# Kernel tuning notes

Measured on AMD Instinct MI355X. Metric: run time of the kernel, lower is better.

The kernel has to match this reference:

```python
import jax, jax.numpy as jnp
import numpy as np

B, D, H, NC = 4096, 128, 4, 10
HD = D // H
EPS = 1e-5


def _ln(x, g, b):
    m = jnp.mean(x, axis=-1, keepdims=True)
    v = jnp.var(x, axis=-1, keepdims=True)
    return (x - m) * jax.lax.rsqrt(v + EPS) * g + b


def _mlp(x, w1, b1, w2, b2):
    h = jax.nn.gelu(x @ w1.T + b1, approximate=False)  # nn.GELU default = exact erf
    return h @ w2.T + b2


def setup_inputs():
    key = jax.random.key(0)
    ks = iter(jax.random.split(key, 40))
    w = lambda *s: jax.random.normal(next(ks), s, dtype=jnp.float32) * 0.02
    inp = {
        'coords': jax.random.uniform(next(ks), (B, 2), dtype=jnp.float32),
        'labels': jax.random.randint(next(ks), (B,), 0, NC),
        'ce_w': w(D, 2), 'ce_b': w(D),
        'emb': w(NC, D),
        'sa_in_w': w(3 * D, D), 'sa_in_b': w(3 * D),
        'sa_out_w': w(D, D), 'sa_out_b': w(D),
        'n1_g': jnp.ones(D), 'n1_b': jnp.zeros(D),
        'm1_w1': w(4 * D, D), 'm1_b1': w(4 * D), 'm1_w2': w(D, 4 * D), 'm1_b2': w(D),
        'n2_g': jnp.ones(D), 'n2_b': jnp.zeros(D),
        'ca_in_w': w(3 * D, D), 'ca_in_b': w(3 * D),
        'ca_out_w': w(D, D), 'ca_out_b': w(D),
        'n3_g': jnp.ones(D), 'n3_b': jnp.zeros(D),
        'm2_w1': w(4 * D, D), 'm2_b1': w(4 * D), 'm2_w2': w(D, 4 * D), 'm2_b2': w(D),
        'n4_g': jnp.ones(D), 'n4_b': jnp.zeros(D),
        'fin_w': w(1, D), 'fin_b': w(1),
    }
    return inp


def reference(coords, labels, ce_w, ce_b, emb, sa_in_w, sa_in_b, sa_out_w, sa_out_b,
              n1_g, n1_b, m1_w1, m1_b1, m1_w2, m1_b2, n2_g, n2_b,
              ca_in_w, ca_in_b, ca_out_w, ca_out_b, n3_g, n3_b,
              m2_w1, m2_b1, m2_w2, m2_b2, n4_g, n4_b, fin_w, fin_b):
    # --- vectorized positional encoding (original loops over batch) ---
    div = 10000.0 ** (2.0 * jnp.arange(D // 2, dtype=jnp.float32) / D)  # [D/2]
    pe_sin = jnp.sin(coords[:, 0:1] / div)  # even slots
    pe_cos = jnp.cos(coords[:, 1:2] / div)  # odd slots
    pe = jnp.stack([pe_sin, pe_cos], axis=-1).reshape(B, D)

    x = coords @ ce_w.T + ce_b + pe  # [B, D]

    # --- self-attention: seq_len = B, batch = 1 (torch seq-first semantics) ---
    qkv = x @ sa_in_w.T + sa_in_b  # [B, 3D]
    q, k, v = jnp.split(qkv, 3, axis=-1)
    q = q.reshape(B, H, HD); k = k.reshape(B, H, HD); v = v.reshape(B, H, HD)
    scores = jnp.einsum('qhd,khd->hqk', q, k) / jnp.sqrt(jnp.float32(HD))  # [H,B,B]
    attn = jax.nn.softmax(scores, axis=-1)
    sa = jnp.einsum('hqk,khd->qhd', attn, v).reshape(B, D) @ sa_out_w.T + sa_out_b

    x = _ln(x + sa, n1_g, n1_b)
    x = _ln(x + _mlp(x, m1_w1, m1_b1, m1_w2, m1_b2), n2_g, n2_b)

    # --- cross-attention: per-sample q_len = kv_len = 1 -> softmax over a
    # single key is exactly 1, so output = out_proj(v_proj(label_emb)) ---
    lab = emb[labels]  # [B, D]
    wv = ca_in_w[2 * D:]; bv = ca_in_b[2 * D:]
    ca = (lab @ wv.T + bv) @ ca_out_w.T + ca_out_b

    x = _ln(x + ca, n3_g, n3_b)
    x = _ln(x + _mlp(x, m2_w1, m2_b1, m2_w2, m2_b2), n4_g, n4_b)

    return jax.nn.sigmoid(x @ fin_w.T + fin_b)  # [B, 1]
```

## Files before the change

kernel.cpp:

```cpp
#include <hip/hip_runtime.h>
#include <hip/hip_bf16.h>


typedef __bf16 bf16_t;
typedef __bf16 bf16x8 __attribute__((ext_vector_type(8)));
typedef __bf16 bf16x4 __attribute__((ext_vector_type(4)));
typedef __bf16 bf16x2 __attribute__((ext_vector_type(2)));
typedef float  f32x4  __attribute__((ext_vector_type(4)));
typedef float  f32x2  __attribute__((ext_vector_type(2)));

__device__ __forceinline__ f32x4 mfma16(bf16x8 a, bf16x8 b, f32x4 c) {
  return __builtin_amdgcn_mfma_f32_16x16x32_bf16(a, b, c, 0, 0, 0);
}

__global__ __launch_bounds__(256) void k_init(const float* __restrict__ coords,
                                              const float* __restrict__ ce_w,
                                              const float* __restrict__ ce_b,
                                              float* __restrict__ xf,
                                              bf16_t* __restrict__ xb,
                                              const float* __restrict__ s0,
                                              const float* __restrict__ s1,
                                              const float* __restrict__ s2,
                                              const float* __restrict__ s3,
                                              const float* __restrict__ s4,
                                              const float* __restrict__ s5,
                                              bf16_t* __restrict__ wdst,
                                              const float* __restrict__ emb,
                                              const float* __restrict__ wvp,
                                              const float* __restrict__ bvp,
                                              const float* __restrict__ cow,
                                              const float* __restrict__ cob,
                                              float* __restrict__ tab) {
  const int bid = blockIdx.x;
  const int tid = threadIdx.x;
  if (bid < 2048) {
    int row = bid * 2 + (tid >> 7);
    int d   = tid & 127;
    float c0 = coords[row * 2 + 0];
    float c1 = coords[row * 2 + 1];
    int   j  = d >> 1;
    float inv = exp2f(-0.20762050593045953f * (float)j);
    float pe  = (d & 1) ? cosf(c1 * inv) : sinf(c0 * inv);
    float x = c0 * ce_w[2 * d] + c1 * ce_w[2 * d + 1] + ce_b[d] + pe;
    xf[(size_t)row * 128 + d] = x;
    xb[(size_t)row * 128 + d] = (bf16_t)x;
  } else if (bid < 2368) {
    int i = (bid - 2048) * 256 + tid;
    const float* src; int off;
    if      (i < 12288) { src = s0; off = i; }
    else if (i < 16384) { src = s1; off = i - 12288; }
    else if (i < 32768) { src = s2; off = i - 16384; }
    else if (i < 49152) { src = s3; off = i - 32768; }
    else if (i < 65536) { src = s4; off = i - 49152; }
    else                { src = s5; off = i - 65536; }
    f32x4 v = *(const f32x4*)(src + (size_t)off * 4);
    bf16x4 o = {(bf16_t)v[0], (bf16_t)v[1], (bf16_t)v[2], (bf16_t)v[3]};
    *(bf16x4*)(wdst + (size_t)i * 4) = o;
  } else {
    __shared__ float embs[10][128];
    __shared__ float t1[10][128];
    for (int i = tid; i < 1280; i += 256) embs[i >> 7][i & 127] = emb[i];
    __syncthreads();
    for (int o = tid; o < 1280; o += 256) {
      int c = o >> 7, n = o & 127;
      float acc = bvp[n];
      const float* wr = wvp + n * 128;
      for (int k2 = 0; k2 < 128; k2++) acc += embs[c][k2] * wr[k2];
      t1[c][n] = acc;
    }
    __syncthreads();
    for (int o = tid; o < 1280; o += 256) {
      int c = o >> 7, dd = o & 127;
      float acc = cob[dd];
      const float* wr = cow + dd * 128;
      for (int n = 0; n < 128; n++) acc += t1[c][n] * wr[n];
      tab[o] = acc;
    }
  }
}

enum { EPI_BF16 = 1, EPI_GELU_BF16 = 2 };

template <int K, int EPI>
__global__ __launch_bounds__(256) void k_gemm(const bf16_t* __restrict__ X,
                                              const bf16_t* __restrict__ Wb,
                                              const float* __restrict__ bias,
                                              bf16_t* __restrict__ outB,
                                              bf16_t* __restrict__ vTout,
                                              int N) {
  const int tid  = threadIdx.x;
  const int lane = tid & 63;
  const int wv   = tid >> 6;
  const int l15  = lane & 15;
  const int quad = lane >> 4;
  const int xbase = blockIdx.x * 64 + (wv >> 1) * 32;
  const int wbase = blockIdx.y * 64 + (wv & 1) * 32;

  const bf16_t* wr0 = Wb + (size_t)(wbase + l15) * K + quad * 8;
  const bf16_t* xr0 = X  + (size_t)(xbase + l15) * K + quad * 8;

  f32x4 acc[2][2];
  const f32x4 zero4 = {0.f, 0.f, 0.f, 0.f};
  for (int i = 0; i < 2; i++)
    for (int t = 0; t < 2; t++) acc[i][t] = zero4;

#pragma unroll 4
  for (int kk = 0; kk < K; kk += 32) {
    bf16x8 a0 = *(const bf16x8*)(wr0 + kk);
    bf16x8 a1 = *(const bf16x8*)(wr0 + 16 * K + kk);
    bf16x8 b0 = *(const bf16x8*)(xr0 + kk);
    bf16x8 b1 = *(const bf16x8*)(xr0 + 16 * K + kk);
    acc[0][0] = mfma16(a0, b0, acc[0][0]);
    acc[0][1] = mfma16(a0, b1, acc[0][1]);
    acc[1][0] = mfma16(a1, b0, acc[1][0]);
    acc[1][1] = mfma16(a1, b1, acc[1][1]);
  }

  f32x4 bv[2];
  bv[0] = *(const f32x4*)(bias + wbase + quad * 4);
  bv[1] = *(const f32x4*)(bias + wbase + 16 + quad * 4);
#pragma unroll
  for (int t = 0; t < 2; t++) {
    int row = xbase + t * 16 + l15;
#pragma unroll
    for (int i = 0; i < 2; i++) {
      int col0 = wbase + i * 16 + quad * 4;
      f32x4 v = acc[i][t] + bv[i];
      if (EPI == EPI_GELU_BF16) {
#pragma unroll
        for (int r = 0; r < 4; r++)
          v[r] = 0.5f * v[r] * (1.0f + erff(v[r] * 0.70710678118654752f));
      }
      bf16x4 o = {(bf16_t)v[0], (bf16_t)v[1], (bf16_t)v[2], (bf16_t)v[3]};
      *(bf16x4*)(outB + (size_t)row * N + col0) = o;
      if (vTout && col0 >= 256) {
#pragma unroll
        for (int r = 0; r < 4; r++)
          vTout[(size_t)(col0 - 256 + r) * 4096 + row] = (bf16_t)v[r];
      }
    }
  }
}

template <int K, int MODE>
__global__ __launch_bounds__(256) void k_gemmln(const bf16_t* __restrict__ X,
                                                const bf16_t* __restrict__ Wb,
                                                const float* __restrict__ bias,
                                                const float* __restrict__ resid,
                                                const float* __restrict__ g1,
                                                const float* __restrict__ b1,
                                                const int* __restrict__ labels,
                                                const float* __restrict__ tab,
                                                const float* __restrict__ g2,
                                                const float* __restrict__ b2,
                                                const float* __restrict__ fw,
                                                const float* __restrict__ fb,
                                                float* __restrict__ xf_out,
                                                bf16_t* __restrict__ xb_out,
                                                float* __restrict__ out) {
  __shared__ float red[2][64][2];

  const int tid  = threadIdx.x;
  const int lane = tid & 63;
  const int wv   = tid >> 6;
  const int l15  = lane & 15;
  const int quad = lane >> 4;
  const int rhalf = wv >> 1, chalf = wv & 1;
  const int rb = blockIdx.x * 64 + rhalf * 32;
  const int cb = chalf * 64;

  const bf16_t* xr0 = X  + (size_t)(rb + l15) * K + quad * 8;
  const bf16_t* wr0 = Wb + (size_t)(cb + l15) * K + quad * 8;

  f32x4 acc[2][4];
  const f32x4 zero4 = {0.f, 0.f, 0.f, 0.f};
  for (int t = 0; t < 2; t++)
    for (int i = 0; i < 4; i++) acc[t][i] = zero4;

#pragma unroll 4
  for (int kk = 0; kk < K; kk += 32) {
    bf16x8 b0 = *(const bf16x8*)(xr0 + kk);
    bf16x8 b1 = *(const bf16x8*)(xr0 + 16 * K + kk);
#pragma unroll
    for (int i = 0; i < 4; i++) {
      bf16x8 a = *(const bf16x8*)(wr0 + (size_t)i * 16 * K + kk);
      acc[0][i] = mfma16(a, b0, acc[0][i]);
      acc[1][i] = mfma16(a, b1, acc[1][i]);
    }
  }

  f32x4 v[2][4];
  float s[2] = {0.f, 0.f}, sq[2] = {0.f, 0.f};
#pragma unroll
  for (int t = 0; t < 2; t++) {
    int row = rb + t * 16 + l15;
#pragma unroll
    for (int i = 0; i < 4; i++) {
      int c = cb + i * 16 + quad * 4;
      f32x4 vv = acc[t][i] + *(const f32x4*)(bias + c)
               + *(const f32x4*)(resid + (size_t)row * 128 + c);
      v[t][i] = vv;
      s[t]  += (vv[0] + vv[1]) + (vv[2] + vv[3]);
      sq[t] += (vv[0] * vv[0] + vv[1] * vv[1]) + (vv[2] * vv[2] + vv[3] * vv[3]);
    }
  }
#pragma unroll
  for (int t = 0; t < 2; t++) {
    s[t]  += __shfl_xor(s[t], 16, 64);  s[t]  += __shfl_xor(s[t], 32, 64);
    sq[t] += __shfl_xor(sq[t], 16, 64); sq[t] += __shfl_xor(sq[t], 32, 64);
    if (quad == 0) {
      red[0][rhalf * 32 + t * 16 + l15][chalf] = s[t];
      red[1][rhalf * 32 + t * 16 + l15][chalf] = sq[t];
    }
  }
  __syncthreads();
  float mean[2], rstd[2];
#pragma unroll
  for (int t = 0; t < 2; t++) {
    int rl = rhalf * 32 + t * 16 + l15;
    float S  = red[0][rl][0] + red[0][rl][1];
    float SQ = red[1][rl][0] + red[1][rl][1];
    mean[t] = S * (1.0f / 128.0f);
    rstd[t] = rsqrtf(SQ * (1.0f / 128.0f) - mean[t] * mean[t] + 1e-5f);
  }

  f32x4 g4[4], b4[4];
#pragma unroll
  for (int i = 0; i < 4; i++) {
    int c = cb + i * 16 + quad * 4;
    g4[i] = *(const f32x4*)(g1 + c);
    b4[i] = *(const f32x4*)(b1 + c);
  }

  if (MODE == 0) {
#pragma unroll
    for (int t = 0; t < 2; t++) {
      int row = rb + t * 16 + l15;
#pragma unroll
      for (int i = 0; i < 4; i++) {
        int c = cb + i * 16 + quad * 4;
        f32x4 y = (v[t][i] - mean[t]) * rstd[t] * g4[i] + b4[i];
        *(f32x4*)(xf_out + (size_t)row * 128 + c) = y;
        bf16x4 o = {(bf16_t)y[0], (bf16_t)y[1], (bf16_t)y[2], (bf16_t)y[3]};
        *(bf16x4*)(xb_out + (size_t)row * 128 + c) = o;
      }
    }
  } else if (MODE == 1) {
    int lab[2];
    float s2v[2] = {0.f, 0.f}, sq2[2] = {0.f, 0.f};
#pragma unroll
    for (int t = 0; t < 2; t++) {
      lab[t] = labels[rb + t * 16 + l15];
#pragma unroll
      for (int i = 0; i < 4; i++) {
        int c = cb + i * 16 + quad * 4;
        f32x4 y = (v[t][i] - mean[t]) * rstd[t] * g4[i] + b4[i];
        y = y + *(const f32x4*)(tab + (size_t)lab[t] * 128 + c);
        v[t][i] = y;
        s2v[t] += (y[0] + y[1]) + (y[2] + y[3]);
        sq2[t] += (y[0] * y[0] + y[1] * y[1]) + (y[2] * y[2] + y[3] * y[3]);
      }
    }
    __syncthreads();
#pragma unroll
    for (int t = 0; t < 2; t++) {
      s2v[t] += __shfl_xor(s2v[t], 16, 64); s2v[t] += __shfl_xor(s2v[t], 32, 64);
      sq2[t] += __shfl_xor(sq2[t], 16, 64); sq2[t] += __shfl_xor(sq2[t], 32, 64);
      if (quad == 0) {
        red[0][rhalf * 32 + t * 16 + l15][chalf] = s2v[t];
        red[1][rhalf * 32 + t * 16 + l15][chalf] = sq2[t];
      }
    }
    __syncthreads();
#pragma unroll
    for (int t = 0; t < 2; t++) {
      int rl = rhalf * 32 + t * 16 + l15;
      float S  = red[0][rl][0] + red[0][rl][1];
      float SQ = red[1][rl][0] + red[1][rl][1];
      mean[t] = S * (1.0f / 128.0f);
      rstd[t] = rsqrtf(SQ * (1.0f / 128.0f) - mean[t] * mean[t] + 1e-5f);
    }
#pragma unroll
    for (int t = 0; t < 2; t++) {
      int row = rb + t * 16 + l15;
#pragma unroll
      for (int i = 0; i < 4; i++) {
        int c = cb + i * 16 + quad * 4;
        f32x4 y = (v[t][i] - mean[t]) * rstd[t] * (*(const f32x4*)(g2 + c))
                + *(const f32x4*)(b2 + c);
        *(f32x4*)(xf_out + (size_t)row * 128 + c) = y;
        bf16x4 o = {(bf16_t)y[0], (bf16_t)y[1], (bf16_t)y[2], (bf16_t)y[3]};
        *(bf16x4*)(xb_out + (size_t)row * 128 + c) = o;
      }
    }
  } else {
    float dot[2] = {0.f, 0.f};
#pragma unroll
    for (int t = 0; t < 2; t++) {
#pragma unroll
      for (int i = 0; i < 4; i++) {
        int c = cb + i * 16 + quad * 4;
        f32x4 y = (v[t][i] - mean[t]) * rstd[t] * g4[i] + b4[i];
        f32x4 fw4 = *(const f32x4*)(fw + c);
        dot[t] += (y[0] * fw4[0] + y[1] * fw4[1]) + (y[2] * fw4[2] + y[3] * fw4[3]);
      }
    }
    __syncthreads();
#pragma unroll
    for (int t = 0; t < 2; t++) {
      dot[t] += __shfl_xor(dot[t], 16, 64); dot[t] += __shfl_xor(dot[t], 32, 64);
      if (quad == 0) red[0][rhalf * 32 + t * 16 + l15][chalf] = dot[t];
    }
    __syncthreads();
    if (chalf == 0 && quad == 0) {
      float fbv = fb[0];
#pragma unroll
      for (int t = 0; t < 2; t++) {
        int rl = rhalf * 32 + t * 16 + l15;
        float logit = red[0][rl][0] + red[0][rl][1] + fbv;
        out[blockIdx.x * 64 + rl] = 1.0f / (1.0f + expf(-logit));
      }
    }
  }
}

__global__ __launch_bounds__(256, 4) void k_attn(const bf16_t* __restrict__ qkv,
                                                 const bf16_t* __restrict__ vT,
                                                 bf16_t* __restrict__ opart,
                                                 float* __restrict__ lpart) {
  __shared__ bf16_t kbuf[128][36];
  __shared__ bf16_t vbuf[32][136];
  __shared__ bf16_t pt[4][2][16][72];

  const int tid  = threadIdx.x;
  const int lane = tid & 63;
  const int wv   = tid >> 6;
  const int l15  = lane & 15;
  const int quad = lane >> 4;
  const int blk  = blockIdx.x;
  const int h    = blk & 3;
  const int ks   = (blk >> 2) & 7;
  const int qt   = (blk >> 5) * 4 + wv;
  const int q0   = qt * 32;
  const int kb   = ks * 512;
  const int task = (qt * 8 + ks) * 4 + h;

  bf16x8 qfA, qfB;
  {
    bf16x8 ra = *(const bf16x8*)(qkv + (size_t)(q0 + l15) * 384 + h * 32 + quad * 8);
    bf16x8 rb = *(const bf16x8*)(qkv + (size_t)(q0 + 16 + l15) * 384 + h * 32 + quad * 8);
#pragma unroll
    for (int j = 0; j < 8; j++) {
      qfA[j] = (bf16_t)((float)ra[j] * 0.17677669529663687f);
      qfB[j] = (bf16_t)((float)rb[j] * 0.17677669529663687f);
    }
  }

  const f32x4 zero4 = {0.f, 0.f, 0.f, 0.f};
  f32x4 oA0 = zero4, oA1 = zero4, oB0 = zero4, oB1 = zero4;
  float laccA = 0.f, laccB = 0.f;

  for (int kk = 0; kk < 512; kk += 128) {
    __syncthreads();
#pragma unroll
    for (int rep = 0; rep < 2; rep++) {
      int idx = rep * 256 + tid;
      int row = idx >> 2, seg = idx & 3;
      bf16x8 t8 = *(const bf16x8*)(qkv + (size_t)(kb + kk + row) * 384
                                   + 128 + h * 32 + seg * 8);
      *(bf16x8*)&kbuf[row][seg * 8] = t8;
      int dim = idx >> 4, vseg = idx & 15;
      bf16x8 v8 = *(const bf16x8*)(vT + (size_t)(h * 32 + dim) * 4096
                                   + kb + kk + vseg * 8);
      *(bf16x8*)&vbuf[dim][vseg * 8] = v8;
    }
    __syncthreads();

#pragma unroll
    for (int half = 0; half < 2; half++) {
      const int ko = half * 64;
      bf16x8 kf0 = *(const bf16x8*)&kbuf[ko + l15][quad * 8];
      bf16x8 kf1 = *(const bf16x8*)&kbuf[ko + 16 + l15][quad * 8];
      bf16x8 kf2 = *(const bf16x8*)&kbuf[ko + 32 + l15][quad * 8];
      bf16x8 kf3 = *(const bf16x8*)&kbuf[ko + 48 + l15][quad * 8];

      f32x4 sA[4], sB[4];
      sA[0] = mfma16(kf0, qfA, zero4);
      sA[1] = mfma16(kf1, qfA, zero4);
      sA[2] = mfma16(kf2, qfA, zero4);
      sA[3] = mfma16(kf3, qfA, zero4);
      sB[0] = mfma16(kf0, qfB, zero4);
      sB[1] = mfma16(kf1, qfB, zero4);
      sB[2] = mfma16(kf2, qfB, zero4);
      sB[3] = mfma16(kf3, qfB, zero4);

#pragma unroll
      for (int t = 0; t < 4; t++) {
        float a0 = __expf(sA[t][0]), a1 = __expf(sA[t][1]);
        float a2 = __expf(sA[t][2]), a3 = __expf(sA[t][3]);
        laccA += (a0 + a1) + (a2 + a3);
        bf16x4 pa = {(bf16_t)a0, (bf16_t)a1, (bf16_t)a2, (bf16_t)a3};
        *(bf16x4*)&pt[wv][0][l15][t * 16 + quad * 4] = pa;
        float b0 = __expf(sB[t][0]), b1 = __expf(sB[t][1]);
        float b2 = __expf(sB[t][2]), b3 = __expf(sB[t][3]);
        laccB += (b0 + b1) + (b2 + b3);
        bf16x4 pb = {(bf16_t)b0, (bf16_t)b1, (bf16_t)b2, (bf16_t)b3};
        *(bf16x4*)&pt[wv][1][l15][t * 16 + quad * 4] = pb;
      }

      bf16x8 pA0 = *(const bf16x8*)&pt[wv][0][l15][quad * 8];
      bf16x8 pA1 = *(const bf16x8*)&pt[wv][0][l15][32 + quad * 8];
      bf16x8 pB0 = *(const bf16x8*)&pt[wv][1][l15][quad * 8];
      bf16x8 pB1 = *(const bf16x8*)&pt[wv][1][l15][32 + quad * 8];

      bf16x8 v00 = *(const bf16x8*)&vbuf[l15][ko + quad * 8];
      bf16x8 v01 = *(const bf16x8*)&vbuf[16 + l15][ko + quad * 8];
      bf16x8 v10 = *(const bf16x8*)&vbuf[l15][ko + 32 + quad * 8];
      bf16x8 v11 = *(const bf16x8*)&vbuf[16 + l15][ko + 32 + quad * 8];

      oA0 = mfma16(pA0, v00, oA0);
      oA0 = mfma16(pA1, v10, oA0);
      oA1 = mfma16(pA0, v01, oA1);
      oA1 = mfma16(pA1, v11, oA1);
      oB0 = mfma16(pB0, v00, oB0);
      oB0 = mfma16(pB1, v10, oB0);
      oB1 = mfma16(pB0, v01, oB1);
      oB1 = mfma16(pB1, v11, oB1);
    }
  }

  laccA += __shfl_xor(laccA, 16, 64); laccA += __shfl_xor(laccA, 32, 64);
  laccB += __shfl_xor(laccB, 16, 64); laccB += __shfl_xor(laccB, 32, 64);
  if (quad == 0) {
    lpart[task * 32 + l15]      = laccA;
    lpart[task * 32 + 16 + l15] = laccB;
  }

  size_t ob = (size_t)task * 1024;
#pragma unroll
  for (int r = 0; r < 4; r++) {
    int qa = quad * 4 + r;
    opart[ob + qa * 32 + l15]             = (bf16_t)oA0[r];
    opart[ob + qa * 32 + 16 + l15]        = (bf16_t)oA1[r];
    opart[ob + (16 + qa) * 32 + l15]      = (bf16_t)oB0[r];
    opart[ob + (16 + qa) * 32 + 16 + l15] = (bf16_t)oB1[r];
  }
}

__global__ __launch_bounds__(256) void k_attn_fin(const bf16_t* __restrict__ opart,
                                                  const float* __restrict__ lpart,
                                                  bf16_t* __restrict__ attnb) {
  int idx = blockIdx.x * 256 + threadIdx.x;
  int d  = idx & 31;
  int q  = (idx >> 5) & 4095;
  int h  = idx >> 17;
  int qt = q >> 5, ql = q & 31;
  float O = 0.f, L = 0.f;
#pragma unroll
  for (int ks = 0; ks < 8; ks++) {
    int t = (qt * 8 + ks) * 4 + h;
    O += (float)opart[(size_t)t * 1024 + ql * 32 + d];
    L += lpart[t * 32 + ql];
  }
  attnb[(size_t)q * 128 + h * 32 + d] = (bf16_t)(O / L);
}

extern "C" void kernel_launch(void* const* d_in, const int* in_sizes, int n_in,
                              void* d_out, int out_size, void* d_ws, size_t ws_size,
                              hipStream_t stream) {
  const float* coords  = (const float*)d_in[0];
  const int*   labels  = (const int*)d_in[1];
  const float* ce_w    = (const float*)d_in[2];
  const float* ce_b    = (const float*)d_in[3];
  const float* emb     = (const float*)d_in[4];
  const float* sa_in_w = (const float*)d_in[5];
  const float* sa_in_b = (const float*)d_in[6];
  const float* sa_out_w= (const float*)d_in[7];
  const float* sa_out_b= (const float*)d_in[8];
  const float* n1_g    = (const float*)d_in[9];
  const float* n1_b    = (const float*)d_in[10];
  const float* m1_w1   = (const float*)d_in[11];
  const float* m1_b1   = (const float*)d_in[12];
  const float* m1_w2   = (const float*)d_in[13];
  const float* m1_b2   = (const float*)d_in[14];
  const float* n2_g    = (const float*)d_in[15];
  const float* n2_b    = (const float*)d_in[16];
  const float* ca_in_w = (const float*)d_in[17];
  const float* ca_in_b = (const float*)d_in[18];
  const float* ca_out_w= (const float*)d_in[19];
  const float* ca_out_b= (const float*)d_in[20];
  const float* n3_g    = (const float*)d_in[21];
  const float* n3_b    = (const float*)d_in[22];
  const float* m2_w1   = (const float*)d_in[23];
  const float* m2_b1   = (const float*)d_in[24];
  const float* m2_w2   = (const float*)d_in[25];
  const float* m2_b2   = (const float*)d_in[26];
  const float* n4_g    = (const float*)d_in[27];
  const float* n4_b    = (const float*)d_in[28];
  const float* fin_w   = (const float*)d_in[29];
  const float* fin_b   = (const float*)d_in[30];
  float* outp = (float*)d_out;

  char* w = (char*)d_ws;
  float*  xf    = (float*)(w);
  float*  tab   = (float*)(w + 2097152);
  bf16_t* wsb   = (bf16_t*)(w + 2105344);
  bf16_t* xb    = (bf16_t*)(w + 2760704);
  bf16_t* attnb = (bf16_t*)(w + 3809280);
  bf16_t* qkvb  = (bf16_t*)(w + 4857856);
  bf16_t* vT    = (bf16_t*)(w + 8003584);
  bf16_t* opart = (bf16_t*)(w + 9052160);
  bf16_t* h1b   = (bf16_t*)(w + 9052160);
  float*  lpart = (float*)(w + 17440768);

  bf16_t* w_sain  = wsb;
  bf16_t* w_saout = wsb + 49152;
  bf16_t* w_m1w1  = wsb + 65536;
  bf16_t* w_m1w2  = wsb + 131072;
  bf16_t* w_m2w1  = wsb + 196608;
  bf16_t* w_m2w2  = wsb + 262144;

  k_init<<<2369, 256, 0, stream>>>(coords, ce_w, ce_b, xf, xb,
                                   sa_in_w, sa_out_w, m1_w1, m1_w2, m2_w1, m2_w2,
                                   wsb, emb, ca_in_w + 256 * 128, ca_in_b + 256,
                                   ca_out_w, ca_out_b, tab);
  k_gemm<128, EPI_BF16><<<dim3(64, 6), 256, 0, stream>>>(xb, w_sain, sa_in_b,
                                                         qkvb, vT, 384);
  k_attn<<<1024, 256, 0, stream>>>(qkvb, vT, opart, lpart);
  k_attn_fin<<<2048, 256, 0, stream>>>(opart, lpart, attnb);
  k_gemmln<128, 0><<<64, 256, 0, stream>>>(attnb, w_saout, sa_out_b, xf,
                                           n1_g, n1_b, nullptr, nullptr,
                                           nullptr, nullptr, nullptr, nullptr,
                                           xf, xb, nullptr);
  k_gemm<128, EPI_GELU_BF16><<<dim3(64, 8), 256, 0, stream>>>(xb, w_m1w1, m1_b1,
                                                              h1b, nullptr, 512);
  k_gemmln<512, 1><<<64, 256, 0, stream>>>(h1b, w_m1w2, m1_b2, xf,
                                           n2_g, n2_b, labels, tab,
                                           n3_g, n3_b, nullptr, nullptr,
                                           xf, xb, nullptr);
  k_gemm<128, EPI_GELU_BF16><<<dim3(64, 8), 256, 0, stream>>>(xb, w_m2w1, m2_b1,
                                                              h1b, nullptr, 512);
  k_gemmln<512, 2><<<64, 256, 0, stream>>>(h1b, w_m2w2, m2_b2, xf,
                                           n4_g, n4_b, nullptr, nullptr,
                                           nullptr, nullptr, fin_w, fin_b,
                                           nullptr, nullptr, outp);

  (void)in_sizes; (void)n_in; (void)out_size; (void)ws_size;
}
```

Baseline: 225.5 us.

## Fuse post-attention out-proj, both MLPs and layernorms into one tail kernel

Replaces five launches (out-proj+LN, two GELU GEMMs, two down-proj+LN kernels) with a single k_tail kernel. Each block handles 16 rows and keeps the activations and the 512-wide hidden layer in shared memory. This removes the global round trips of the intermediate activations and the launch gaps between the stages. In exchange there are only 256 blocks with 16-row tiles, so every block rereads all the weights from global/L2 and MFMA reuse per weight load is lower.

```diff
diff --git a/kernel.cpp b/kernel.cpp
--- a/kernel.cpp
+++ b/kernel.cpp
@@ -142,188 +142,6 @@
   }
 }
 
-template <int K, int MODE>
-__global__ __launch_bounds__(256) void k_gemmln(const bf16_t* __restrict__ X,
-                                                const bf16_t* __restrict__ Wb,
-                                                const float* __restrict__ bias,
-                                                const float* __restrict__ resid,
-                                                const float* __restrict__ g1,
-                                                const float* __restrict__ b1,
-                                                const int* __restrict__ labels,
-                                                const float* __restrict__ tab,
-                                                const float* __restrict__ g2,
-                                                const float* __restrict__ b2,
-                                                const float* __restrict__ fw,
-                                                const float* __restrict__ fb,
-                                                float* __restrict__ xf_out,
-                                                bf16_t* __restrict__ xb_out,
-                                                float* __restrict__ out) {
-  __shared__ float red[2][64][2];
-
-  const int tid  = threadIdx.x;
-  const int lane = tid & 63;
-  const int wv   = tid >> 6;
-  const int l15  = lane & 15;
-  const int quad = lane >> 4;
-  const int rhalf = wv >> 1, chalf = wv & 1;
-  const int rb = blockIdx.x * 64 + rhalf * 32;
-  const int cb = chalf * 64;
-
-  const bf16_t* xr0 = X  + (size_t)(rb + l15) * K + quad * 8;
-  const bf16_t* wr0 = Wb + (size_t)(cb + l15) * K + quad * 8;
-
-  f32x4 acc[2][4];
-  const f32x4 zero4 = {0.f, 0.f, 0.f, 0.f};
-  for (int t = 0; t < 2; t++)
-    for (int i = 0; i < 4; i++) acc[t][i] = zero4;
-
-#pragma unroll 4
-  for (int kk = 0; kk < K; kk += 32) {
-    bf16x8 b0 = *(const bf16x8*)(xr0 + kk);
-    bf16x8 b1 = *(const bf16x8*)(xr0 + 16 * K + kk);
-#pragma unroll
-    for (int i = 0; i < 4; i++) {
-      bf16x8 a = *(const bf16x8*)(wr0 + (size_t)i * 16 * K + kk);
-      acc[0][i] = mfma16(a, b0, acc[0][i]);
-      acc[1][i] = mfma16(a, b1, acc[1][i]);
-    }
-  }
-
-  f32x4 v[2][4];
-  float s[2] = {0.f, 0.f}, sq[2] = {0.f, 0.f};
-#pragma unroll
-  for (int t = 0; t < 2; t++) {
-    int row = rb + t * 16 + l15;
-#pragma unroll
-    for (int i = 0; i < 4; i++) {
-      int c = cb + i * 16 + quad * 4;
-      f32x4 vv = acc[t][i] + *(const f32x4*)(bias + c)
-               + *(const f32x4*)(resid + (size_t)row * 128 + c);
-      v[t][i] = vv;
-      s[t]  += (vv[0] + vv[1]) + (vv[2] + vv[3]);
-      sq[t] += (vv[0] * vv[0] + vv[1] * vv[1]) + (vv[2] * vv[2] + vv[3] * vv[3]);
-    }
-  }
-#pragma unroll
-  for (int t = 0; t < 2; t++) {
-    s[t]  += __shfl_xor(s[t], 16, 64);  s[t]  += __shfl_xor(s[t], 32, 64);
-    sq[t] += __shfl_xor(sq[t], 16, 64); sq[t] += __shfl_xor(sq[t], 32, 64);
-    if (quad == 0) {
-      red[0][rhalf * 32 + t * 16 + l15][chalf] = s[t];
-      red[1][rhalf * 32 + t * 16 + l15][chalf] = sq[t];
-    }
-  }
-  __syncthreads();
-  float mean[2], rstd[2];
-#pragma unroll
-  for (int t = 0; t < 2; t++) {
-    int rl = rhalf * 32 + t * 16 + l15;
-    float S  = red[0][rl][0] + red[0][rl][1];
-    float SQ = red[1][rl][0] + red[1][rl][1];
-    mean[t] = S * (1.0f / 128.0f);
-    rstd[t] = rsqrtf(SQ * (1.0f / 128.0f) - mean[t] * mean[t] + 1e-5f);
-  }
-
-  f32x4 g4[4], b4[4];
-#pragma unroll
-  for (int i = 0; i < 4; i++) {
-    int c = cb + i * 16 + quad * 4;
-    g4[i] = *(const f32x4*)(g1 + c);
-    b4[i] = *(const f32x4*)(b1 + c);
-  }
-
-  if (MODE == 0) {
-#pragma unroll
-    for (int t = 0; t < 2; t++) {
-      int row = rb + t * 16 + l15;
-#pragma unroll
-      for (int i = 0; i < 4; i++) {
-        int c = cb + i * 16 + quad * 4;
-        f32x4 y = (v[t][i] - mean[t]) * rstd[t] * g4[i] + b4[i];
-        *(f32x4*)(xf_out + (size_t)row * 128 + c) = y;
-        bf16x4 o = {(bf16_t)y[0], (bf16_t)y[1], (bf16_t)y[2], (bf16_t)y[3]};
-        *(bf16x4*)(xb_out + (size_t)row * 128 + c) = o;
-      }
-    }
-  } else if (MODE == 1) {
-    int lab[2];
-    float s2v[2] = {0.f, 0.f}, sq2[2] = {0.f, 0.f};
-#pragma unroll
-    for (int t = 0; t < 2; t++) {
-      lab[t] = labels[rb + t * 16 + l15];
-#pragma unroll
-      for (int i = 0; i < 4; i++) {
-        int c = cb + i * 16 + quad * 4;
-        f32x4 y = (v[t][i] - mean[t]) * rstd[t] * g4[i] + b4[i];
-        y = y + *(const f32x4*)(tab + (size_t)lab[t] * 128 + c);
-        v[t][i] = y;
-        s2v[t] += (y[0] + y[1]) + (y[2] + y[3]);
-        sq2[t] += (y[0] * y[0] + y[1] * y[1]) + (y[2] * y[2] + y[3] * y[3]);
-      }
-    }
-    __syncthreads();
-#pragma unroll
-    for (int t = 0; t < 2; t++) {
-      s2v[t] += __shfl_xor(s2v[t], 16, 64); s2v[t] += __shfl_xor(s2v[t], 32, 64);
-      sq2[t] += __shfl_xor(sq2[t], 16, 64); sq2[t] += __shfl_xor(sq2[t], 32, 64);
-      if (quad == 0) {
-        red[0][rhalf * 32 + t * 16 + l15][chalf] = s2v[t];
-        red[1][rhalf * 32 + t * 16 + l15][chalf] = sq2[t];
-      }
-    }
-    __syncthreads();
-#pragma unroll
-    for (int t = 0; t < 2; t++) {
-      int rl = rhalf * 32 + t * 16 + l15;
-      float S  = red[0][rl][0] + red[0][rl][1];
-      float SQ = red[1][rl][0] + red[1][rl][1];
-      mean[t] = S * (1.0f / 128.0f);
-      rstd[t] = rsqrtf(SQ * (1.0f / 128.0f) - mean[t] * mean[t] + 1e-5f);
-    }
-#pragma unroll
-    for (int t = 0; t < 2; t++) {
-      int row = rb + t * 16 + l15;
-#pragma unroll
-      for (int i = 0; i < 4; i++) {
-        int c = cb + i * 16 + quad * 4;
-        f32x4 y = (v[t][i] - mean[t]) * rstd[t] * (*(const f32x4*)(g2 + c))
-                + *(const f32x4*)(b2 + c);
-        *(f32x4*)(xf_out + (size_t)row * 128 + c) = y;
-        bf16x4 o = {(bf16_t)y[0], (bf16_t)y[1], (bf16_t)y[2], (bf16_t)y[3]};
-        *(bf16x4*)(xb_out + (size_t)row * 128 + c) = o;
-      }
-    }
-  } else {
-    float dot[2] = {0.f, 0.f};
-#pragma unroll
-    for (int t = 0; t < 2; t++) {
-#pragma unroll
-      for (int i = 0; i < 4; i++) {
-        int c = cb + i * 16 + quad * 4;
-        f32x4 y = (v[t][i] - mean[t]) * rstd[t] * g4[i] + b4[i];
-        f32x4 fw4 = *(const f32x4*)(fw + c);
-        dot[t] += (y[0] * fw4[0] + y[1] * fw4[1]) + (y[2] * fw4[2] + y[3] * fw4[3]);
-      }
-    }
-    __syncthreads();
-#pragma unroll
-    for (int t = 0; t < 2; t++) {
-      dot[t] += __shfl_xor(dot[t], 16, 64); dot[t] += __shfl_xor(dot[t], 32, 64);
-      if (quad == 0) red[0][rhalf * 32 + t * 16 + l15][chalf] = dot[t];
-    }
-    __syncthreads();
-    if (chalf == 0 && quad == 0) {
-      float fbv = fb[0];
-#pragma unroll
-      for (int t = 0; t < 2; t++) {
-        int rl = rhalf * 32 + t * 16 + l15;
-        float logit = red[0][rl][0] + red[0][rl][1] + fbv;
-        out[blockIdx.x * 64 + rl] = 1.0f / (1.0f + expf(-logit));
-      }
-    }
-  }
-}
-
 __global__ __launch_bounds__(256, 4) void k_attn(const bf16_t* __restrict__ qkv,
                                                  const bf16_t* __restrict__ vT,
                                                  bf16_t* __restrict__ opart,
@@ -463,6 +281,197 @@
     L += lpart[t * 32 + ql];
   }
   attnb[(size_t)q * 128 + h * 32 + d] = (bf16_t)(O / L);
+}
+
+__global__ __launch_bounds__(512) void k_tail(
+    const bf16_t* __restrict__ attnb, const float* __restrict__ xf,
+    const bf16_t* __restrict__ wso, const float* __restrict__ bso,
+    const float* __restrict__ n1g, const float* __restrict__ n1b,
+    const bf16_t* __restrict__ w11, const float* __restrict__ b11,
+    const bf16_t* __restrict__ w12, const float* __restrict__ b12,
+    const float* __restrict__ n2g, const float* __restrict__ n2b,
+    const int* __restrict__ labels, const float* __restrict__ tab,
+    const float* __restrict__ n3g, const float* __restrict__ n3b,
+    const bf16_t* __restrict__ w21, const float* __restrict__ b21,
+    const bf16_t* __restrict__ w22, const float* __restrict__ b22,
+    const float* __restrict__ n4g, const float* __restrict__ n4b,
+    const float* __restrict__ fw, const float* __restrict__ fb,
+    float* __restrict__ out) {
+  __shared__ float  xs[16][132];
+  __shared__ bf16_t xsb[16][136];
+  __shared__ bf16_t hb[16][520];
+  __shared__ float  red[2][16][8];
+
+  const int tid  = threadIdx.x;
+  const int lane = tid & 63;
+  const int wv   = tid >> 6;
+  const int l15  = lane & 15;
+  const int quad = lane >> 4;
+  const int row  = blockIdx.x * 16 + l15;
+  const int cb1  = wv * 16;
+  const int c1   = cb1 + quad * 4;
+  const int cb4  = wv * 64;
+
+  const f32x4 zero4 = {0.f, 0.f, 0.f, 0.f};
+
+  {
+    f32x4 acc = zero4;
+    const bf16_t* br = attnb + (size_t)row * 128 + quad * 8;
+    const bf16_t* ar = wso + (size_t)(cb1 + l15) * 128 + quad * 8;
+#pragma unroll
+    for (int kk = 0; kk < 128; kk += 32)
+      acc = mfma16(*(const bf16x8*)(ar + kk), *(const bf16x8*)(br + kk), acc);
+
+    f32x4 v = acc + *(const f32x4*)(bso + c1)
+                  + *(const f32x4*)(xf + (size_t)row * 128 + c1);
+    float s  = (v[0] + v[1]) + (v[2] + v[3]);
+    float sq = (v[0]*v[0] + v[1]*v[1]) + (v[2]*v[2] + v[3]*v[3]);
+    s  += __shfl_xor(s, 16, 64);  s  += __shfl_xor(s, 32, 64);
+    sq += __shfl_xor(sq, 16, 64); sq += __shfl_xor(sq, 32, 64);
+    if (quad == 0) { red[0][l15][wv] = s; red[1][l15][wv] = sq; }
+    __syncthreads();
+    float S = 0.f, SQ = 0.f;
+#pragma unroll
+    for (int w2 = 0; w2 < 8; w2++) { S += red[0][l15][w2]; SQ += red[1][l15][w2]; }
+    float mean = S * (1.f / 128.f);
+    float rstd = rsqrtf(SQ * (1.f / 128.f) - mean * mean + 1e-5f);
+    f32x4 y = (v - mean) * rstd * (*(const f32x4*)(n1g + c1))
+            + *(const f32x4*)(n1b + c1);
+    *(f32x4*)&xs[l15][c1] = y;
+    bf16x4 o = {(bf16_t)y[0], (bf16_t)y[1], (bf16_t)y[2], (bf16_t)y[3]};
+    *(bf16x4*)&xsb[l15][c1] = o;
+  }
+  __syncthreads();
+
+  {
+    f32x4 au[4] = {zero4, zero4, zero4, zero4};
+#pragma unroll
+    for (int kk = 0; kk < 128; kk += 32) {
+      bf16x8 bfr = *(const bf16x8*)&xsb[l15][kk + quad * 8];
+#pragma unroll
+      for (int i = 0; i < 4; i++) {
+        bf16x8 a = *(const bf16x8*)(w11 + (size_t)(cb4 + i * 16 + l15) * 128
+                                    + kk + quad * 8);
+        au[i] = mfma16(a, bfr, au[i]);
+      }
+    }
+#pragma unroll
+    for (int i = 0; i < 4; i++) {
+      int c = cb4 + i * 16 + quad * 4;
+      f32x4 vv = au[i] + *(const f32x4*)(b11 + c);
+#pragma unroll
+      for (int r = 0; r < 4; r++)
+        vv[r] = 0.5f * vv[r] * (1.0f + erff(vv[r] * 0.70710678118654752f));
+      bf16x4 o = {(bf16_t)vv[0], (bf16_t)vv[1], (bf16_t)vv[2], (bf16_t)vv[3]};
+      *(bf16x4*)&hb[l15][c] = o;
+    }
+  }
+  __syncthreads();
+
+  {
+    f32x4 acc = zero4;
+    const bf16_t* ar = w12 + (size_t)(cb1 + l15) * 512 + quad * 8;
+#pragma unroll 4
+    for (int kk = 0; kk < 512; kk += 32) {
+      bf16x8 bfr = *(const bf16x8*)&hb[l15][kk + quad * 8];
+      acc = mfma16(*(const bf16x8*)(ar + kk), bfr, acc);
+    }
+    f32x4 v = acc + *(const f32x4*)(b12 + c1) + *(const f32x4*)&xs[l15][c1];
+    float s  = (v[0] + v[1]) + (v[2] + v[3]);
+    float sq = (v[0]*v[0] + v[1]*v[1]) + (v[2]*v[2] + v[3]*v[3]);
+    s  += __shfl_xor(s, 16, 64);  s  += __shfl_xor(s, 32, 64);
+    sq += __shfl_xor(sq, 16, 64); sq += __shfl_xor(sq, 32, 64);
+    if (quad == 0) { red[0][l15][wv] = s; red[1][l15][wv] = sq; }
+    __syncthreads();
+    float S = 0.f, SQ = 0.f;
+#pragma unroll
+    for (int w2 = 0; w2 < 8; w2++) { S += red[0][l15][w2]; SQ += red[1][l15][w2]; }
+    float mean = S * (1.f / 128.f);
+    float rstd = rsqrtf(SQ * (1.f / 128.f) - mean * mean + 1e-5f);
+    int lab = labels[row];
+    f32x4 y = (v - mean) * rstd * (*(const f32x4*)(n2g + c1))
+            + *(const f32x4*)(n2b + c1)
+            + *(const f32x4*)(tab + (size_t)lab * 128 + c1);
+    float s3  = (y[0] + y[1]) + (y[2] + y[3]);
+    float sq3 = (y[0]*y[0] + y[1]*y[1]) + (y[2]*y[2] + y[3]*y[3]);
+    s3  += __shfl_xor(s3, 16, 64);  s3  += __shfl_xor(s3, 32, 64);
+    sq3 += __shfl_xor(sq3, 16, 64); sq3 += __shfl_xor(sq3, 32, 64);
+    __syncthreads();
+    if (quad == 0) { red[0][l15][wv] = s3; red[1][l15][wv] = sq3; }
+    __syncthreads();
+    float S3 = 0.f, SQ3 = 0.f;
+#pragma unroll
+    for (int w2 = 0; w2 < 8; w2++) { S3 += red[0][l15][w2]; SQ3 += red[1][l15][w2]; }
+    float mean3 = S3 * (1.f / 128.f);
+    float rstd3 = rsqrtf(SQ3 * (1.f / 128.f) - mean3 * mean3 + 1e-5f);
+    f32x4 y3 = (y - mean3) * rstd3 * (*(const f32x4*)(n3g + c1))
+             + *(const f32x4*)(n3b + c1);
+    *(f32x4*)&xs[l15][c1] = y3;
+    bf16x4 o = {(bf16_t)y3[0], (bf16_t)y3[1], (bf16_t)y3[2], (bf16_t)y3[3]};
+    *(bf16x4*)&xsb[l15][c1] = o;
+  }
+  __syncthreads();
+
+  {
+    f32x4 au[4] = {zero4, zero4, zero4, zero4};
+#pragma unroll
+    for (int kk = 0; kk < 128; kk += 32) {
+      bf16x8 bfr = *(const bf16x8*)&xsb[l15][kk + quad * 8];
+#pragma unroll
+      for (int i = 0; i < 4; i++) {
+        bf16x8 a = *(const bf16x8*)(w21 + (size_t)(cb4 + i * 16 + l15) * 128
+                                    + kk + quad * 8);
+        au[i] = mfma16(a, bfr, au[i]);
+      }
+    }
+#pragma unroll
+    for (int i = 0; i < 4; i++) {
+      int c = cb4 + i * 16 + quad * 4;
+      f32x4 vv = au[i] + *(const f32x4*)(b21 + c);
+#pragma unroll
+      for (int r = 0; r < 4; r++)
+        vv[r] = 0.5f * vv[r] * (1.0f + erff(vv[r] * 0.70710678118654752f));
+      bf16x4 o = {(bf16_t)vv[0], (bf16_t)vv[1], (bf16_t)vv[2], (bf16_t)vv[3]};
+      *(bf16x4*)&hb[l15][c] = o;
+    }
+  }
+  __syncthreads();
+
+  {
+    f32x4 acc = zero4;
+    const bf16_t* ar = w22 + (size_t)(cb1 + l15) * 512 + quad * 8;
+#pragma unroll 4
+    for (int kk = 0; kk < 512; kk += 32) {
+      bf16x8 bfr = *(const bf16x8*)&hb[l15][kk + quad * 8];
+      acc = mfma16(*(const bf16x8*)(ar + kk), bfr, acc);
+    }
+    f32x4 v = acc + *(const f32x4*)(b22 + c1) + *(const f32x4*)&xs[l15][c1];
+    float s  = (v[0] + v[1]) + (v[2] + v[3]);
+    float sq = (v[0]*v[0] + v[1]*v[1]) + (v[2]*v[2] + v[3]*v[3]);
+    s  += __shfl_xor(s, 16, 64);  s  += __shfl_xor(s, 32, 64);
+    sq += __shfl_xor(sq, 16, 64); sq += __shfl_xor(sq, 32, 64);
+    if (quad == 0) { red[0][l15][wv] = s; red[1][l15][wv] = sq; }
+    __syncthreads();
+    float S = 0.f, SQ = 0.f;
+#pragma unroll
+    for (int w2 = 0; w2 < 8; w2++) { S += red[0][l15][w2]; SQ += red[1][l15][w2]; }
+    float mean = S * (1.f / 128.f);
+    float rstd = rsqrtf(SQ * (1.f / 128.f) - mean * mean + 1e-5f);
+    f32x4 y = (v - mean) * rstd * (*(const f32x4*)(n4g + c1))
+            + *(const f32x4*)(n4b + c1);
+    f32x4 fwv = *(const f32x4*)(fw + c1);
+    float dot = (y[0]*fwv[0] + y[1]*fwv[1]) + (y[2]*fwv[2] + y[3]*fwv[3]);
+    dot += __shfl_xor(dot, 16, 64); dot += __shfl_xor(dot, 32, 64);
+    __syncthreads();
+    if (quad == 0) red[0][l15][wv] = dot;
+    __syncthreads();
+    if (wv == 0 && quad == 0) {
+      float logit = fb[0];
+#pragma unroll
+      for (int w2 = 0; w2 < 8; w2++) logit += red[0][l15][w2];
+      out[row] = 1.0f / (1.0f + expf(-logit));
+    }
+  }
 }
 
 extern "C" void kernel_launch(void* const* d_in, const int* in_sizes, int n_in,
@@ -510,7 +519,6 @@
   bf16_t* qkvb  = (bf16_t*)(w + 4857856);
   bf16_t* vT    = (bf16_t*)(w + 8003584);
   bf16_t* opart = (bf16_t*)(w + 9052160);
-  bf16_t* h1b   = (bf16_t*)(w + 9052160);
   float*  lpart = (float*)(w + 17440768);
 
   bf16_t* w_sain  = wsb;
@@ -528,22 +536,12 @@
                                                          qkvb, vT, 384);
   k_attn<<<1024, 256, 0, stream>>>(qkvb, vT, opart, lpart);
   k_attn_fin<<<2048, 256, 0, stream>>>(opart, lpart, attnb);
-  k_gemmln<128, 0><<<64, 256, 0, stream>>>(attnb, w_saout, sa_out_b, xf,
-                                           n1_g, n1_b, nullptr, nullptr,
-                                           nullptr, nullptr, nullptr, nullptr,
-                                           xf, xb, nullptr);
-  k_gemm<128, EPI_GELU_BF16><<<dim3(64, 8), 256, 0, stream>>>(xb, w_m1w1, m1_b1,
-                                                              h1b, nullptr, 512);
-  k_gemmln<512, 1><<<64, 256, 0, stream>>>(h1b, w_m1w2, m1_b2, xf,
-                                           n2_g, n2_b, labels, tab,
-                                           n3_g, n3_b, nullptr, nullptr,
-                                           xf, xb, nullptr);
-  k_gemm<128, EPI_GELU_BF16><<<dim3(64, 8), 256, 0, stream>>>(xb, w_m2w1, m2_b1,
-                                                              h1b, nullptr, 512);
-  k_gemmln<512, 2><<<64, 256, 0, stream>>>(h1b, w_m2w2, m2_b2, xf,
-                                           n4_g, n4_b, nullptr, nullptr,
-                                           nullptr, nullptr, fin_w, fin_b,
-                                           nullptr, nullptr, outp);
+  k_tail<<<256, 512, 0, stream>>>(attnb, xf,
+                                  w_saout, sa_out_b, n1_g, n1_b,
+                                  w_m1w1, m1_b1, w_m1w2, m1_b2, n2_g, n2_b,
+                                  labels, tab, n3_g, n3_b,
+                                  w_m2w1, m2_b1, w_m2w2, m2_b2, n4_g, n4_b,
+                                  fin_w, fin_b, outp);
 
   (void)in_sizes; (void)n_in; (void)out_size; (void)ws_size;
 }
```

New measurement: 192.6 us. 1.17x faster.
